# Performance work log

Hardware: AMD Instinct MI355X
Metric: run time of the kernel (lower is better)

## Reference

```python
import jax, jax.numpy as jnp
import numpy as np

D_MODEL = 1024
N_HEADS = 8
HEAD_DIM = D_MODEL // N_HEADS
B, T = 4, 2048


def setup_inputs() -> dict:
    key = jax.random.key(0)
    ks = jax.random.split(key, 10)
    x = jax.random.normal(ks[0], (B, T, D_MODEL), dtype=jnp.float32)
    # causal mask: True entries are masked (matches torch masked_fill semantics)
    mask = jnp.triu(jnp.ones((T, T), dtype=bool), k=1)

    def xavier(k, shape):
        fan_in, fan_out = shape[1], shape[0]
        lim = float(np.sqrt(6.0 / (fan_in + fan_out)))
        return jax.random.uniform(k, shape, jnp.float32, -lim, lim)

    Wq = xavier(ks[1], (D_MODEL, D_MODEL)); bq = jnp.zeros((D_MODEL,), jnp.float32)
    Wk = xavier(ks[2], (D_MODEL, D_MODEL)); bk = jnp.zeros((D_MODEL,), jnp.float32)
    Wv = xavier(ks[3], (D_MODEL, D_MODEL)); bv = jnp.zeros((D_MODEL,), jnp.float32)
    Wo = xavier(ks[4], (D_MODEL, D_MODEL)); bo = jnp.zeros((D_MODEL,), jnp.float32)
    return {"x": x, "mask": mask, "Wq": Wq, "bq": bq, "Wk": Wk, "bk": bk,
            "Wv": Wv, "bv": bv, "Wo": Wo, "bo": bo}


def reference(x, mask, Wq, bq, Wk, bk, Wv, bv, Wo, bo):
    Bsz, Tlen, _ = x.shape
    # torch Linear: y = x @ W.T + b
    Q = (x @ Wq.T + bq).reshape(Bsz, Tlen, N_HEADS, HEAD_DIM).transpose(0, 2, 1, 3)  # [B,H,T,Dh]
    K = (x @ Wk.T + bk).reshape(Bsz, Tlen, N_HEADS, HEAD_DIM).transpose(0, 2, 1, 3)  # [B,H,T,Dh]
    V_shared = x @ Wv.T + bv  # [B,T,D] shared across heads
    scale = 1.0 / jnp.sqrt(jnp.float32(HEAD_DIM))
    scores = jnp.einsum('bhqd,bhkd->bhqk', Q, K) * scale  # [B,H,T,T]
    scores = jnp.where(mask[None, None, :, :], jnp.float32(-1e9), scores)
    attn_per_head = jax.nn.softmax(scores, axis=-1)
    alpha_agg = attn_per_head.mean(axis=1)  # [B,T,T] head-averaged attention
    out = jnp.einsum('bqk,bkd->bqd', alpha_agg, V_shared) @ Wo.T + bo
    return out, alpha_agg
```

## Files before the change

### kernel.cpp

```cpp
#include <hip/hip_runtime.h>
#include <hip/hip_bf16.h>

#define D_MODEL 1024
#define NH 8
#define HD 128
#define BATCH 4
#define TSEQ 2048
#define MROWS (BATCH * TSEQ)
#define QKV_LD 3072

typedef __attribute__((ext_vector_type(8))) __bf16 bf16x8;
typedef __attribute__((ext_vector_type(4))) __bf16 bf16x4;
typedef __attribute__((ext_vector_type(4))) float f32x4;
typedef __attribute__((ext_vector_type(8))) unsigned short u16x8;

#define SC2 0.1275174441680632f

__device__ __forceinline__ void gload16(const void* g, void* lds) {
  __builtin_amdgcn_global_load_lds(
      (const __attribute__((address_space(1))) unsigned int*)g,
      (__attribute__((address_space(3))) unsigned int*)lds, 16, 0, 0);
}

__global__ __launch_bounds__(256) void cvt_f32_to_bf16(const float* __restrict__ in,
                                                       __bf16* __restrict__ out, int n4) {
  int i = blockIdx.x * 256 + threadIdx.x;
  if (i < n4) {
    float4 v = reinterpret_cast<const float4*>(in)[i];
    bf16x4 o;
    o[0] = (__bf16)v.x; o[1] = (__bf16)v.y; o[2] = (__bf16)v.z; o[3] = (__bf16)v.w;
    reinterpret_cast<bf16x4*>(out)[i] = o;
  }
}

__global__ __launch_bounds__(256) void cvt4_weights(const float* __restrict__ w0,
                                                    const float* __restrict__ w1,
                                                    const float* __restrict__ w2,
                                                    const float* __restrict__ w3,
                                                    __bf16* __restrict__ out) {
  const int per = D_MODEL * D_MODEL / 4;
  int i = blockIdx.x * 256 + threadIdx.x;
  int m = i / per, j = i - m * per;
  const float* src = (m == 0) ? w0 : (m == 1) ? w1 : (m == 2) ? w2 : w3;
  float4 v = reinterpret_cast<const float4*>(src)[j];
  bf16x4 o;
  o[0] = (__bf16)v.x; o[1] = (__bf16)v.y; o[2] = (__bf16)v.z; o[3] = (__bf16)v.w;
  reinterpret_cast<bf16x4*>(out)[i] = o;
}

__global__ __launch_bounds__(256) void concat_bias(const float* __restrict__ a,
                                                   const float* __restrict__ b,
                                                   const float* __restrict__ c,
                                                   float* __restrict__ o) {
  int i = blockIdx.x * 256 + threadIdx.x;
  if (i < 3072) o[i] = (i < 1024) ? a[i] : (i < 2048) ? b[i - 1024] : c[i - 2048];
}

__global__ __launch_bounds__(256) void invert_lsum(float* __restrict__ L, int n) {
  int i = blockIdx.x * 256 + threadIdx.x;
  if (i < n) L[i] = 1.0f / (8.0f * L[i]);
}

template <bool BF16OUT, bool CAUSAL, bool AFP32>
__global__ __launch_bounds__(256) void gemm128(const void* __restrict__ Aip,
                                               const __bf16* __restrict__ Bp,
                                               const float* __restrict__ bias,
                                               void* __restrict__ Yp, int K, int ldy,
                                               size_t sA, size_t sB, size_t sY) {
  __shared__ __bf16 As[2][128 * 32];
  __shared__ __bf16 Bs[2][128 * 32];
  const int tid = threadIdx.x;
  const int w = tid >> 6, l = tid & 63;
  const int lr = l & 15, lg = l >> 4;
  const int m0 = blockIdx.y * 128, n0 = blockIdx.x * 128;
  const int z = blockIdx.z;
  const __bf16* Ab = AFP32 ? nullptr : (const __bf16*)Aip + z * sA;
  const float* Af = AFP32 ? (const float*)Aip + z * sA : nullptr;
  const __bf16* Bb = Bp + z * sB;
  const int wm = w >> 1, wn = w & 1;
  f32x4 acc[4][4] = {};
  const int Klim = CAUSAL ? (m0 + 128 < K ? m0 + 128 : K) : K;
  const int nt = Klim >> 5;

  auto stage = [&](int t, int buf) {
    const int k0 = t << 5;
    if constexpr (!AFP32) {
#pragma unroll
      for (int i = 0; i < 2; ++i) {
        int s = w * 128 + i * 64 + l;
        int row = s >> 2, scp = s & 3;
        int sc = scp ^ ((row >> 1) & 3);
        gload16(Ab + (size_t)(m0 + row) * K + k0 + sc * 8, (char*)As[buf] + s * 16);
      }
    } else {
#pragma unroll
      for (int i = 0; i < 2; ++i) {
        int s = w * 128 + i * 64 + l;
        int row = s >> 2, sc = s & 3;
        const float* src = Af + (size_t)(m0 + row) * K + k0 + sc * 8;
        float4 lo = *reinterpret_cast<const float4*>(src);
        float4 hi = *reinterpret_cast<const float4*>(src + 4);
        bf16x8 v;
        v[0] = (__bf16)lo.x; v[1] = (__bf16)lo.y; v[2] = (__bf16)lo.z; v[3] = (__bf16)lo.w;
        v[4] = (__bf16)hi.x; v[5] = (__bf16)hi.y; v[6] = (__bf16)hi.z; v[7] = (__bf16)hi.w;
        int p = row * 4 + (sc ^ ((row >> 1) & 3));
        *reinterpret_cast<bf16x8*>((char*)As[buf] + p * 16) = v;
      }
    }
#pragma unroll
    for (int i = 0; i < 2; ++i) {
      int s = w * 128 + i * 64 + l;
      int row = s >> 2, scp = s & 3;
      int sc = scp ^ ((row >> 1) & 3);
      gload16(Bb + (size_t)(n0 + row) * K + k0 + sc * 8, (char*)Bs[buf] + s * 16);
    }
  };

  stage(0, 0);
  __syncthreads();
  int cur = 0;
  for (int t = 0; t < nt; ++t) {
    if (t + 1 < nt) stage(t + 1, cur ^ 1);
    bf16x8 af[4], bf[4];
#pragma unroll
    for (int f = 0; f < 4; ++f) {
      int ar = wm * 64 + f * 16 + lr;
      af[f] = *reinterpret_cast<const bf16x8*>((const char*)As[cur] + ar * 64 +
                                               ((lg ^ ((ar >> 1) & 3)) * 16));
      int br = wn * 64 + f * 16 + lr;
      bf[f] = *reinterpret_cast<const bf16x8*>((const char*)Bs[cur] + br * 64 +
                                               ((lg ^ ((br >> 1) & 3)) * 16));
    }
#pragma unroll
    for (int mf = 0; mf < 4; ++mf)
#pragma unroll
      for (int nf = 0; nf < 4; ++nf)
        acc[mf][nf] = __builtin_amdgcn_mfma_f32_16x16x32_bf16(af[mf], bf[nf], acc[mf][nf], 0, 0, 0);
    __syncthreads();
    cur ^= 1;
  }

#pragma unroll
  for (int mf = 0; mf < 4; ++mf) {
#pragma unroll
    for (int nf = 0; nf < 4; ++nf) {
#pragma unroll
      for (int r = 0; r < 4; ++r) {
        int grow = m0 + wm * 64 + mf * 16 + lg * 4 + r;
        int gcol = n0 + wn * 64 + nf * 16 + lr;
        float v = acc[mf][nf][r];
        if (bias) v += bias[gcol];
        if constexpr (BF16OUT)
          ((__bf16*)Yp + z * sY)[(size_t)grow * ldy + gcol] = (__bf16)v;
        else
          ((float*)Yp + z * sY)[(size_t)grow * ldy + gcol] = v;
      }
    }
  }
}

__global__ __launch_bounds__(256) void transpose_v(const __bf16* __restrict__ V,
                                                   __bf16* __restrict__ Vt) {
  __shared__ unsigned short tile[64 * 72];
  const int b = blockIdx.z;
  const int t0 = blockIdx.x * 64, d0 = blockIdx.y * 64;
  const int tid = threadIdx.x;
#pragma unroll
  for (int i = 0; i < 2; ++i) {
    int s = i * 256 + tid;
    int r = s >> 3, c8 = s & 7;
    u16x8 v = *reinterpret_cast<const u16x8*>(V + ((size_t)b * TSEQ + t0 + r) * QKV_LD + d0 + c8 * 8);
    *reinterpret_cast<u16x8*>(&tile[r * 72 + c8 * 8]) = v;
  }
  __syncthreads();
#pragma unroll
  for (int i = 0; i < 2; ++i) {
    int s = i * 256 + tid;
    int dr = s >> 3, t8 = s & 7;
    u16x8 o;
#pragma unroll
    for (int j = 0; j < 8; ++j) o[j] = tile[(t8 * 8 + j) * 72 + dr];
    *reinterpret_cast<u16x8*>(Vt + ((size_t)b * D_MODEL + d0 + dr) * TSEQ + t0 + t8 * 8) = o;
  }
}

__device__ __forceinline__ void stage_tile128(const __bf16* __restrict__ src,
                                              __bf16* __restrict__ dst, int tid, int ld) {
#pragma unroll
  for (int i = 0; i < 4; ++i) {
    int s = i * 512 + tid;
    int row = s >> 4, sp = s & 15;
    int sl = sp ^ (row & 15);
    gload16(src + (size_t)row * ld + sl * 8, (char*)dst + s * 16);
  }
}

__device__ __forceinline__ bf16x8 ldfrag(const __bf16* t, int row, int c, int lg) {
  return *reinterpret_cast<const bf16x8*>((const char*)t + row * 256 +
                                          (((c * 4 + lg) ^ (row & 15)) * 16));
}

template <int MODE>
__global__ __launch_bounds__(512) void attn128(const __bf16* __restrict__ QKV,
                                               const float* __restrict__ Linv,
                                               float* __restrict__ Out) {
  const int kt = blockIdx.x, qt = blockIdx.y, b = blockIdx.z;
  const int tid = threadIdx.x;
  const int q0 = qt * 128, k0 = kt * 128;
  if (kt > qt) {
    if (MODE == 1) {
      float4 zz = {0.f, 0.f, 0.f, 0.f};
#pragma unroll
      for (int i = 0; i < 8; ++i) {
        int s = i * 512 + tid;
        int row = s >> 5, c = s & 31;
        *reinterpret_cast<float4*>(Out + ((size_t)(b * TSEQ) + q0 + row) * TSEQ + k0 + c * 4) = zz;
      }
    }
    return;
  }
  __shared__ __bf16 Qs[2][128 * 128];
  __shared__ __bf16 Ks[2][128 * 128];
  const int w = tid >> 6, l = tid & 63;
  const int lr = l & 15, lg = l >> 4;
  const int wq = w >> 1;
  const int wk = w & 1;
  const __bf16* qb0 = QKV + (size_t)(b * TSEQ + q0) * QKV_LD;
  const __bf16* kb0 = QKV + (size_t)(b * TSEQ + k0) * QKV_LD + 1024;

  stage_tile128(qb0, Qs[0], tid, QKV_LD);
  stage_tile128(kb0, Ks[0], tid, QKV_LD);
  __syncthreads();

  float outv[2][4][4] = {};
  int cur = 0;
  for (int h = 0; h < NH; ++h) {
    if (h + 1 < NH) {
      stage_tile128(qb0 + (h + 1) * HD, Qs[cur ^ 1], tid, QKV_LD);
      stage_tile128(kb0 + (h + 1) * HD, Ks[cur ^ 1], tid, QKV_LD);
    }
    bf16x8 af[2][4], bf[4][4];
#pragma unroll
    for (int mf = 0; mf < 2; ++mf)
#pragma unroll
      for (int c = 0; c < 4; ++c) af[mf][c] = ldfrag(Qs[cur], wq * 32 + mf * 16 + lr, c, lg);
#pragma unroll
    for (int nf = 0; nf < 4; ++nf)
#pragma unroll
      for (int c = 0; c < 4; ++c) bf[nf][c] = ldfrag(Ks[cur], wk * 64 + nf * 16 + lr, c, lg);
    f32x4 acc[2][4] = {};
#pragma unroll
    for (int c = 0; c < 4; ++c)
#pragma unroll
      for (int mf = 0; mf < 2; ++mf)
#pragma unroll
        for (int nf = 0; nf < 4; ++nf)
          acc[mf][nf] = __builtin_amdgcn_mfma_f32_16x16x32_bf16(af[mf][c], bf[nf][c], acc[mf][nf], 0, 0, 0);

    if constexpr (MODE == 0) {
      float ls[2][4] = {};
#pragma unroll
      for (int mf = 0; mf < 2; ++mf)
#pragma unroll
        for (int nf = 0; nf < 4; ++nf)
#pragma unroll
          for (int r = 0; r < 4; ++r) {
            int q = q0 + wq * 32 + mf * 16 + lg * 4 + r;
            int k = k0 + wk * 64 + nf * 16 + lr;
            if (kt < qt || k <= q) ls[mf][r] += exp2f(acc[mf][nf][r] * SC2);
          }
#pragma unroll
      for (int m = 1; m < 16; m <<= 1)
#pragma unroll
        for (int mf = 0; mf < 2; ++mf)
#pragma unroll
          for (int r = 0; r < 4; ++r) ls[mf][r] += __shfl_xor(ls[mf][r], m, 64);
      if (lr == 0) {
#pragma unroll
        for (int mf = 0; mf < 2; ++mf)
#pragma unroll
          for (int r = 0; r < 4; ++r)
            atomicAdd(&Out[((size_t)(b * NH + h)) * TSEQ + q0 + wq * 32 + mf * 16 + lg * 4 + r],
                      ls[mf][r]);
      }
    } else {
      float4 li[2];
#pragma unroll
      for (int mf = 0; mf < 2; ++mf)
        li[mf] = *reinterpret_cast<const float4*>(
            &Linv[((size_t)(b * NH + h)) * TSEQ + q0 + wq * 32 + mf * 16 + lg * 4]);
#pragma unroll
      for (int mf = 0; mf < 2; ++mf)
#pragma unroll
        for (int nf = 0; nf < 4; ++nf)
#pragma unroll
          for (int r = 0; r < 4; ++r) {
            int q = q0 + wq * 32 + mf * 16 + lg * 4 + r;
            int k = k0 + wk * 64 + nf * 16 + lr;
            if (kt < qt || k <= q)
              outv[mf][nf][r] += exp2f(acc[mf][nf][r] * SC2) * (&li[mf].x)[r];
          }
    }
    __syncthreads();
    cur ^= 1;
  }
  if constexpr (MODE == 1) {
#pragma unroll
    for (int mf = 0; mf < 2; ++mf)
#pragma unroll
      for (int nf = 0; nf < 4; ++nf)
#pragma unroll
        for (int r = 0; r < 4; ++r)
          Out[((size_t)(b * TSEQ) + q0 + wq * 32 + mf * 16 + lg * 4 + r) * TSEQ +
              k0 + wk * 64 + nf * 16 + lr] = outv[mf][nf][r];
  }
}

extern "C" void kernel_launch(void* const* d_in, const int* in_sizes, int n_in,
                              void* d_out, int out_size, void* d_ws, size_t ws_size,
                              hipStream_t stream) {
  const float* x  = (const float*)d_in[0];
  const float* Wq = (const float*)d_in[2];
  const float* bq = (const float*)d_in[3];
  const float* Wk = (const float*)d_in[4];
  const float* bk = (const float*)d_in[5];
  const float* Wv = (const float*)d_in[6];
  const float* bv = (const float*)d_in[7];
  const float* Wo = (const float*)d_in[8];
  const float* bo = (const float*)d_in[9];

  float* out_f = (float*)d_out;
  float* alpha = out_f + (size_t)MROWS * D_MODEL;

  char* p = (char*)d_ws;
  __bf16* xb   = (__bf16*)p; p += (size_t)MROWS * D_MODEL * 2;
  __bf16* wqb  = (__bf16*)p; p += (size_t)D_MODEL * D_MODEL * 2;
  __bf16* wkb  = (__bf16*)p; p += (size_t)D_MODEL * D_MODEL * 2;
  __bf16* wvb  = (__bf16*)p; p += (size_t)D_MODEL * D_MODEL * 2;
  __bf16* wob  = (__bf16*)p; p += (size_t)D_MODEL * D_MODEL * 2;
  __bf16* qkv  = (__bf16*)p; p += (size_t)MROWS * QKV_LD * 2;
  __bf16* vtb  = (__bf16*)p; p += (size_t)BATCH * D_MODEL * TSEQ * 2;
  float* lsum  = (float*)p;  p += (size_t)BATCH * NH * TSEQ * 4;
  float* bcat  = (float*)p;  p += 3072 * 4;
  __bf16* midb = xb;

  hipMemsetAsync(lsum, 0, (size_t)BATCH * NH * TSEQ * 4, stream);

  {
    int n4 = MROWS * D_MODEL / 4;
    cvt_f32_to_bf16<<<n4 / 256, 256, 0, stream>>>(x, xb, n4);
    int w4 = 4 * D_MODEL * D_MODEL / 4;
    cvt4_weights<<<w4 / 256, 256, 0, stream>>>(Wq, Wk, Wv, Wo, wqb);
    concat_bias<<<12, 256, 0, stream>>>(bq, bk, bv, bcat);
  }

  gemm128<true, false, false><<<dim3(QKV_LD / 128, MROWS / 128), 256, 0, stream>>>(
      xb, wqb, bcat, qkv, D_MODEL, QKV_LD, 0, 0, 0);

  transpose_v<<<dim3(TSEQ / 64, D_MODEL / 64, BATCH), 256, 0, stream>>>(qkv + 2048, vtb);

  attn128<0><<<dim3(TSEQ / 128, TSEQ / 128, BATCH), 512, 0, stream>>>(qkv, nullptr, lsum);
  invert_lsum<<<(BATCH * NH * TSEQ) / 256, 256, 0, stream>>>(lsum, BATCH * NH * TSEQ);

  attn128<1><<<dim3(TSEQ / 128, TSEQ / 128, BATCH), 512, 0, stream>>>(qkv, lsum, alpha);

  gemm128<true, true, true><<<dim3(D_MODEL / 128, TSEQ / 128, BATCH), 256, 0, stream>>>(
      alpha, vtb, nullptr, midb, TSEQ, D_MODEL,
      (size_t)TSEQ * TSEQ, (size_t)D_MODEL * TSEQ, (size_t)TSEQ * D_MODEL);

  gemm128<false, false, false><<<dim3(D_MODEL / 128, MROWS / 128), 256, 0, stream>>>(
      midb, wob, bo, out_f, D_MODEL, D_MODEL, 0, 0, 0);
}
```

Before: 393.5 us.

## Restructure attention score kernels to 4 waves with 64-wide K-chunk staging

The attention score kernels now run with 256 threads (4 waves) instead of 512. Each wave computes a 64x64 tile, so there are more MFMAs per fragment load. Staging switches from full 128-wide head tiles to 64-column chunks, cutting LDS use from 128KB to 64KB, which may allow more blocks per CU. Accumulators persist across two chunks per head and are reset after the softmax or normalization step. The cost is higher register pressure from the 4x4 accumulators plus the outv array, which could hurt occupancy.

```diff
diff --git a/kernel.cpp b/kernel.cpp
--- a/kernel.cpp
+++ b/kernel.cpp
@@ -184,26 +184,26 @@
   }
 }
 
-__device__ __forceinline__ void stage_tile128(const __bf16* __restrict__ src,
-                                              __bf16* __restrict__ dst, int tid, int ld) {
+__device__ __forceinline__ void stage64(const __bf16* __restrict__ src,
+                                        __bf16* __restrict__ dst, int tid) {
 #pragma unroll
   for (int i = 0; i < 4; ++i) {
-    int s = i * 512 + tid;
-    int row = s >> 4, sp = s & 15;
-    int sl = sp ^ (row & 15);
-    gload16(src + (size_t)row * ld + sl * 8, (char*)dst + s * 16);
-  }
-}
-
-__device__ __forceinline__ bf16x8 ldfrag(const __bf16* t, int row, int c, int lg) {
-  return *reinterpret_cast<const bf16x8*>((const char*)t + row * 256 +
-                                          (((c * 4 + lg) ^ (row & 15)) * 16));
+    int s = i * 256 + tid;
+    int row = s >> 3, sp = s & 7;
+    int sl = sp ^ (row & 7);
+    gload16(src + (size_t)row * QKV_LD + sl * 8, (char*)dst + s * 16);
+  }
+}
+
+__device__ __forceinline__ bf16x8 ldfrag64(const __bf16* t, int row, int c, int lg) {
+  return *reinterpret_cast<const bf16x8*>((const char*)t + row * 128 +
+                                          (((c * 4 + lg) ^ (row & 7)) * 16));
 }
 
 template <int MODE>
-__global__ __launch_bounds__(512) void attn128(const __bf16* __restrict__ QKV,
-                                               const float* __restrict__ Linv,
-                                               float* __restrict__ Out) {
+__global__ __launch_bounds__(256) void attn4w(const __bf16* __restrict__ QKV,
+                                              const float* __restrict__ Linv,
+                                              float* __restrict__ Out) {
   const int kt = blockIdx.x, qt = blockIdx.y, b = blockIdx.z;
   const int tid = threadIdx.x;
   const int q0 = qt * 128, k0 = kt * 128;
@@ -211,107 +211,115 @@
     if (MODE == 1) {
       float4 zz = {0.f, 0.f, 0.f, 0.f};
 #pragma unroll
-      for (int i = 0; i < 8; ++i) {
-        int s = i * 512 + tid;
+      for (int i = 0; i < 16; ++i) {
+        int s = i * 256 + tid;
         int row = s >> 5, c = s & 31;
         *reinterpret_cast<float4*>(Out + ((size_t)(b * TSEQ) + q0 + row) * TSEQ + k0 + c * 4) = zz;
       }
     }
     return;
   }
-  __shared__ __bf16 Qs[2][128 * 128];
-  __shared__ __bf16 Ks[2][128 * 128];
+  __shared__ __bf16 Qs[2][128 * 64];
+  __shared__ __bf16 Ks[2][128 * 64];
   const int w = tid >> 6, l = tid & 63;
   const int lr = l & 15, lg = l >> 4;
-  const int wq = w >> 1;
-  const int wk = w & 1;
+  const int wq = w >> 1, wk = w & 1;
   const __bf16* qb0 = QKV + (size_t)(b * TSEQ + q0) * QKV_LD;
   const __bf16* kb0 = QKV + (size_t)(b * TSEQ + k0) * QKV_LD + 1024;
 
-  stage_tile128(qb0, Qs[0], tid, QKV_LD);
-  stage_tile128(kb0, Ks[0], tid, QKV_LD);
+  stage64(qb0, Qs[0], tid);
+  stage64(kb0, Ks[0], tid);
   __syncthreads();
 
-  float outv[2][4][4] = {};
+  f32x4 acc[4][4] = {};
+  float outv[4][4][4] = {};
+  float li[4][4];
   int cur = 0;
-  for (int h = 0; h < NH; ++h) {
-    if (h + 1 < NH) {
-      stage_tile128(qb0 + (h + 1) * HD, Qs[cur ^ 1], tid, QKV_LD);
-      stage_tile128(kb0 + (h + 1) * HD, Ks[cur ^ 1], tid, QKV_LD);
-    }
-    bf16x8 af[2][4], bf[4][4];
-#pragma unroll
-    for (int mf = 0; mf < 2; ++mf)
-#pragma unroll
-      for (int c = 0; c < 4; ++c) af[mf][c] = ldfrag(Qs[cur], wq * 32 + mf * 16 + lr, c, lg);
-#pragma unroll
-    for (int nf = 0; nf < 4; ++nf)
-#pragma unroll
-      for (int c = 0; c < 4; ++c) bf[nf][c] = ldfrag(Ks[cur], wk * 64 + nf * 16 + lr, c, lg);
-    f32x4 acc[2][4] = {};
-#pragma unroll
-    for (int c = 0; c < 4; ++c)
-#pragma unroll
-      for (int mf = 0; mf < 2; ++mf)
+#pragma unroll 1
+  for (int t = 0; t < 16; ++t) {
+    if (t < 15) {
+      stage64(qb0 + (t + 1) * 64, Qs[cur ^ 1], tid);
+      stage64(kb0 + (t + 1) * 64, Ks[cur ^ 1], tid);
+    }
+    if (MODE == 1 && (t & 1) == 0) {
+      int h = t >> 1;
+#pragma unroll
+      for (int mf = 0; mf < 4; ++mf) {
+        float4 v = *reinterpret_cast<const float4*>(
+            &Linv[((size_t)(b * NH + h)) * TSEQ + q0 + wq * 64 + mf * 16 + lg * 4]);
+        li[mf][0] = v.x; li[mf][1] = v.y; li[mf][2] = v.z; li[mf][3] = v.w;
+      }
+    }
+#pragma unroll
+    for (int c = 0; c < 2; ++c) {
+      bf16x8 af[4], bf[4];
+#pragma unroll
+      for (int f = 0; f < 4; ++f) {
+        af[f] = ldfrag64(Qs[cur], wq * 64 + f * 16 + lr, c, lg);
+        bf[f] = ldfrag64(Ks[cur], wk * 64 + f * 16 + lr, c, lg);
+      }
+#pragma unroll
+      for (int mf = 0; mf < 4; ++mf)
 #pragma unroll
         for (int nf = 0; nf < 4; ++nf)
-          acc[mf][nf] = __builtin_amdgcn_mfma_f32_16x16x32_bf16(af[mf][c], bf[nf][c], acc[mf][nf], 0, 0, 0);
-
-    if constexpr (MODE == 0) {
-      float ls[2][4] = {};
-#pragma unroll
-      for (int mf = 0; mf < 2; ++mf)
-#pragma unroll
-        for (int nf = 0; nf < 4; ++nf)
-#pragma unroll
-          for (int r = 0; r < 4; ++r) {
-            int q = q0 + wq * 32 + mf * 16 + lg * 4 + r;
-            int k = k0 + wk * 64 + nf * 16 + lr;
-            if (kt < qt || k <= q) ls[mf][r] += exp2f(acc[mf][nf][r] * SC2);
-          }
-#pragma unroll
-      for (int m = 1; m < 16; m <<= 1)
-#pragma unroll
-        for (int mf = 0; mf < 2; ++mf)
-#pragma unroll
-          for (int r = 0; r < 4; ++r) ls[mf][r] += __shfl_xor(ls[mf][r], m, 64);
-      if (lr == 0) {
-#pragma unroll
-        for (int mf = 0; mf < 2; ++mf)
-#pragma unroll
-          for (int r = 0; r < 4; ++r)
-            atomicAdd(&Out[((size_t)(b * NH + h)) * TSEQ + q0 + wq * 32 + mf * 16 + lg * 4 + r],
-                      ls[mf][r]);
-      }
-    } else {
-      float4 li[2];
-#pragma unroll
-      for (int mf = 0; mf < 2; ++mf)
-        li[mf] = *reinterpret_cast<const float4*>(
-            &Linv[((size_t)(b * NH + h)) * TSEQ + q0 + wq * 32 + mf * 16 + lg * 4]);
-#pragma unroll
-      for (int mf = 0; mf < 2; ++mf)
-#pragma unroll
-        for (int nf = 0; nf < 4; ++nf)
-#pragma unroll
-          for (int r = 0; r < 4; ++r) {
-            int q = q0 + wq * 32 + mf * 16 + lg * 4 + r;
-            int k = k0 + wk * 64 + nf * 16 + lr;
-            if (kt < qt || k <= q)
-              outv[mf][nf][r] += exp2f(acc[mf][nf][r] * SC2) * (&li[mf].x)[r];
-          }
+          acc[mf][nf] = __builtin_amdgcn_mfma_f32_16x16x32_bf16(af[mf], bf[nf], acc[mf][nf], 0, 0, 0);
+    }
+    if (t & 1) {
+      const int h = t >> 1;
+      const bool diag = (kt == qt);
+      if constexpr (MODE == 0) {
+        float ls[4][4] = {};
+#pragma unroll
+        for (int mf = 0; mf < 4; ++mf)
+#pragma unroll
+          for (int nf = 0; nf < 4; ++nf)
+#pragma unroll
+            for (int r = 0; r < 4; ++r) {
+              int q = wq * 64 + mf * 16 + lg * 4 + r;
+              int k = wk * 64 + nf * 16 + lr;
+              if (!diag || k <= q) ls[mf][r] += exp2f(acc[mf][nf][r] * SC2);
+              acc[mf][nf][r] = 0.f;
+            }
+#pragma unroll
+        for (int m = 1; m < 16; m <<= 1)
+#pragma unroll
+          for (int mf = 0; mf < 4; ++mf)
+#pragma unroll
+            for (int r = 0; r < 4; ++r) ls[mf][r] += __shfl_xor(ls[mf][r], m, 64);
+        if (lr == 0) {
+#pragma unroll
+          for (int mf = 0; mf < 4; ++mf)
+#pragma unroll
+            for (int r = 0; r < 4; ++r)
+              atomicAdd(&Out[((size_t)(b * NH + h)) * TSEQ + q0 + wq * 64 + mf * 16 + lg * 4 + r],
+                        ls[mf][r]);
+        }
+      } else {
+#pragma unroll
+        for (int mf = 0; mf < 4; ++mf)
+#pragma unroll
+          for (int nf = 0; nf < 4; ++nf)
+#pragma unroll
+            for (int r = 0; r < 4; ++r) {
+              int q = wq * 64 + mf * 16 + lg * 4 + r;
+              int k = wk * 64 + nf * 16 + lr;
+              if (!diag || k <= q)
+                outv[mf][nf][r] += exp2f(acc[mf][nf][r] * SC2) * li[mf][r];
+              acc[mf][nf][r] = 0.f;
+            }
+      }
     }
     __syncthreads();
     cur ^= 1;
   }
   if constexpr (MODE == 1) {
 #pragma unroll
-    for (int mf = 0; mf < 2; ++mf)
+    for (int mf = 0; mf < 4; ++mf)
 #pragma unroll
       for (int nf = 0; nf < 4; ++nf)
 #pragma unroll
         for (int r = 0; r < 4; ++r)
-          Out[((size_t)(b * TSEQ) + q0 + wq * 32 + mf * 16 + lg * 4 + r) * TSEQ +
+          Out[((size_t)(b * TSEQ) + q0 + wq * 64 + mf * 16 + lg * 4 + r) * TSEQ +
               k0 + wk * 64 + nf * 16 + lr] = outv[mf][nf][r];
   }
 }
@@ -359,10 +367,10 @@
 
   transpose_v<<<dim3(TSEQ / 64, D_MODEL / 64, BATCH), 256, 0, stream>>>(qkv + 2048, vtb);
 
-  attn128<0><<<dim3(TSEQ / 128, TSEQ / 128, BATCH), 512, 0, stream>>>(qkv, nullptr, lsum);
+  attn4w<0><<<dim3(TSEQ / 128, TSEQ / 128, BATCH), 256, 0, stream>>>(qkv, nullptr, lsum);
   invert_lsum<<<(BATCH * NH * TSEQ) / 256, 256, 0, stream>>>(lsum, BATCH * NH * TSEQ);
 
-  attn128<1><<<dim3(TSEQ / 128, TSEQ / 128, BATCH), 512, 0, stream>>>(qkv, lsum, alpha);
+  attn4w<1><<<dim3(TSEQ / 128, TSEQ / 128, BATCH), 256, 0, stream>>>(qkv, lsum, alpha);
 
   gemm128<true, true, true><<<dim3(D_MODEL / 128, TSEQ / 128, BATCH), 256, 0, stream>>>(
       alpha, vtb, nullptr, midb, TSEQ, D_MODEL,
```

Measured after the change: 510.8 us. +29.8%, slower.

## Stage attention Q/K in 32-wide k-slices to shrink LDS and raise occupancy

Applied to the files above, without the earlier changes.

The attention score kernels now stream Q and K in 32-column slices (one 16-byte load per thread per slice) instead of staging a full 128x128 head tile per head. This cuts shared memory from 128KB to 32KB and sets launch bounds to allow four blocks per CU. Accumulators are carried across four slices per head, and the exp/normalise step runs every fourth iteration. In exchange there are many more barriers (32 per block instead of 8) and less load latency is hidden per stage.

```diff
diff --git a/kernel.cpp b/kernel.cpp
--- a/kernel.cpp
+++ b/kernel.cpp
@@ -184,29 +184,13 @@
   }
 }
 
-__device__ __forceinline__ void stage_tile128(const __bf16* __restrict__ src,
-                                              __bf16* __restrict__ dst, int tid, int ld) {
-#pragma unroll
-  for (int i = 0; i < 4; ++i) {
-    int s = i * 512 + tid;
-    int row = s >> 4, sp = s & 15;
-    int sl = sp ^ (row & 15);
-    gload16(src + (size_t)row * ld + sl * 8, (char*)dst + s * 16);
-  }
-}
-
-__device__ __forceinline__ bf16x8 ldfrag(const __bf16* t, int row, int c, int lg) {
-  return *reinterpret_cast<const bf16x8*>((const char*)t + row * 256 +
-                                          (((c * 4 + lg) ^ (row & 15)) * 16));
-}
-
 template <int MODE>
-__global__ __launch_bounds__(512) void attn128(const __bf16* __restrict__ QKV,
-                                               const float* __restrict__ Linv,
-                                               float* __restrict__ Out) {
+__global__ __launch_bounds__(512, 4) void attn8w(const __bf16* __restrict__ QKV,
+                                                 const float* __restrict__ Linv,
+                                                 float* __restrict__ Out) {
   const int kt = blockIdx.x, qt = blockIdx.y, b = blockIdx.z;
+  const int q0 = qt * 128, k0 = kt * 128;
   const int tid = threadIdx.x;
-  const int q0 = qt * 128, k0 = kt * 128;
   if (kt > qt) {
     if (MODE == 1) {
       float4 zz = {0.f, 0.f, 0.f, 0.f};
@@ -219,100 +203,113 @@
     }
     return;
   }
-  __shared__ __bf16 Qs[2][128 * 128];
-  __shared__ __bf16 Ks[2][128 * 128];
+  __shared__ __bf16 As[2][128 * 32];
+  __shared__ __bf16 Bs[2][128 * 32];
   const int w = tid >> 6, l = tid & 63;
   const int lr = l & 15, lg = l >> 4;
-  const int wq = w >> 1;
-  const int wk = w & 1;
-  const __bf16* qb0 = QKV + (size_t)(b * TSEQ + q0) * QKV_LD;
-  const __bf16* kb0 = QKV + (size_t)(b * TSEQ + k0) * QKV_LD + 1024;
-
-  stage_tile128(qb0, Qs[0], tid, QKV_LD);
-  stage_tile128(kb0, Ks[0], tid, QKV_LD);
+  const int wq = w >> 1, wk = w & 1;
+  const __bf16* Qb = QKV + (size_t)(b * TSEQ + q0) * QKV_LD;
+  const __bf16* Kb = QKV + (size_t)(b * TSEQ + k0) * QKV_LD + 1024;
+  const int srow = tid >> 2, ssl = (tid & 3) ^ ((srow >> 1) & 3);
+  const __bf16* qsrc = Qb + (size_t)srow * QKV_LD + ssl * 8;
+  const __bf16* ksrc = Kb + (size_t)srow * QKV_LD + ssl * 8;
+
+  gload16(qsrc, (char*)As[0] + tid * 16);
+  gload16(ksrc, (char*)Bs[0] + tid * 16);
   __syncthreads();
 
+  f32x4 acc[2][4] = {};
   float outv[2][4][4] = {};
+  const bool diag = (kt == qt);
   int cur = 0;
-  for (int h = 0; h < NH; ++h) {
-    if (h + 1 < NH) {
-      stage_tile128(qb0 + (h + 1) * HD, Qs[cur ^ 1], tid, QKV_LD);
-      stage_tile128(kb0 + (h + 1) * HD, Ks[cur ^ 1], tid, QKV_LD);
-    }
-    bf16x8 af[2][4], bf[4][4];
-#pragma unroll
-    for (int mf = 0; mf < 2; ++mf)
-#pragma unroll
-      for (int c = 0; c < 4; ++c) af[mf][c] = ldfrag(Qs[cur], wq * 32 + mf * 16 + lr, c, lg);
-#pragma unroll
-    for (int nf = 0; nf < 4; ++nf)
-#pragma unroll
-      for (int c = 0; c < 4; ++c) bf[nf][c] = ldfrag(Ks[cur], wk * 64 + nf * 16 + lr, c, lg);
-    f32x4 acc[2][4] = {};
-#pragma unroll
-    for (int c = 0; c < 4; ++c)
-#pragma unroll
-      for (int mf = 0; mf < 2; ++mf)
-#pragma unroll
-        for (int nf = 0; nf < 4; ++nf)
-          acc[mf][nf] = __builtin_amdgcn_mfma_f32_16x16x32_bf16(af[mf][c], bf[nf][c], acc[mf][nf], 0, 0, 0);
-
-    if constexpr (MODE == 0) {
-      float ls[2][4] = {};
-#pragma unroll
-      for (int mf = 0; mf < 2; ++mf)
-#pragma unroll
-        for (int nf = 0; nf < 4; ++nf)
-#pragma unroll
-          for (int r = 0; r < 4; ++r) {
-            int q = q0 + wq * 32 + mf * 16 + lg * 4 + r;
-            int k = k0 + wk * 64 + nf * 16 + lr;
-            if (kt < qt || k <= q) ls[mf][r] += exp2f(acc[mf][nf][r] * SC2);
-          }
-#pragma unroll
-      for (int m = 1; m < 16; m <<= 1)
-#pragma unroll
-        for (int mf = 0; mf < 2; ++mf)
-#pragma unroll
-          for (int r = 0; r < 4; ++r) ls[mf][r] += __shfl_xor(ls[mf][r], m, 64);
-      if (lr == 0) {
-#pragma unroll
-        for (int mf = 0; mf < 2; ++mf)
-#pragma unroll
-          for (int r = 0; r < 4; ++r)
-            atomicAdd(&Out[((size_t)(b * NH + h)) * TSEQ + q0 + wq * 32 + mf * 16 + lg * 4 + r],
-                      ls[mf][r]);
-      }
-    } else {
-      float4 li[2];
-#pragma unroll
-      for (int mf = 0; mf < 2; ++mf)
-        li[mf] = *reinterpret_cast<const float4*>(
-            &Linv[((size_t)(b * NH + h)) * TSEQ + q0 + wq * 32 + mf * 16 + lg * 4]);
-#pragma unroll
-      for (int mf = 0; mf < 2; ++mf)
-#pragma unroll
-        for (int nf = 0; nf < 4; ++nf)
-#pragma unroll
-          for (int r = 0; r < 4; ++r) {
-            int q = q0 + wq * 32 + mf * 16 + lg * 4 + r;
-            int k = k0 + wk * 64 + nf * 16 + lr;
-            if (kt < qt || k <= q)
-              outv[mf][nf][r] += exp2f(acc[mf][nf][r] * SC2) * (&li[mf].x)[r];
-          }
+#pragma unroll 1
+  for (int t = 0; t < 32; ++t) {
+    if (t < 31) {
+      gload16(qsrc + (t + 1) * 32, (char*)As[cur ^ 1] + tid * 16);
+      gload16(ksrc + (t + 1) * 32, (char*)Bs[cur ^ 1] + tid * 16);
+    }
+    bf16x8 af[2], bf[4];
+#pragma unroll
+    for (int f = 0; f < 2; ++f) {
+      int ar = wq * 32 + f * 16 + lr;
+      af[f] = *reinterpret_cast<const bf16x8*>((const char*)As[cur] + ar * 64 +
+                                               ((lg ^ ((ar >> 1) & 3)) * 16));
+    }
+#pragma unroll
+    for (int g = 0; g < 4; ++g) {
+      int br = wk * 64 + g * 16 + lr;
+      bf[g] = *reinterpret_cast<const bf16x8*>((const char*)Bs[cur] + br * 64 +
+                                               ((lg ^ ((br >> 1) & 3)) * 16));
+    }
+#pragma unroll
+    for (int f = 0; f < 2; ++f)
+#pragma unroll
+      for (int g = 0; g < 4; ++g)
+        acc[f][g] = __builtin_amdgcn_mfma_f32_16x16x32_bf16(af[f], bf[g], acc[f][g], 0, 0, 0);
+
+    if ((t & 3) == 3) {
+      const int h = t >> 2;
+      if constexpr (MODE == 0) {
+        float ls[2][4] = {};
+#pragma unroll
+        for (int f = 0; f < 2; ++f)
+#pragma unroll
+          for (int g = 0; g < 4; ++g)
+#pragma unroll
+            for (int r = 0; r < 4; ++r) {
+              int q = wq * 32 + f * 16 + lg * 4 + r;
+              int k = wk * 64 + g * 16 + lr;
+              if (!diag || k <= q) ls[f][r] += exp2f(acc[f][g][r] * SC2);
+              acc[f][g][r] = 0.f;
+            }
+#pragma unroll
+        for (int m = 1; m < 16; m <<= 1)
+#pragma unroll
+          for (int f = 0; f < 2; ++f)
+#pragma unroll
+            for (int r = 0; r < 4; ++r) ls[f][r] += __shfl_xor(ls[f][r], m, 64);
+        if (lr == 0) {
+#pragma unroll
+          for (int f = 0; f < 2; ++f)
+#pragma unroll
+            for (int r = 0; r < 4; ++r)
+              atomicAdd(&Out[((size_t)(b * NH + h)) * TSEQ + q0 + wq * 32 + f * 16 + lg * 4 + r],
+                        ls[f][r]);
+        }
+      } else {
+        float li[2][4];
+#pragma unroll
+        for (int f = 0; f < 2; ++f) {
+          float4 v = *reinterpret_cast<const float4*>(
+              &Linv[((size_t)(b * NH + h)) * TSEQ + q0 + wq * 32 + f * 16 + lg * 4]);
+          li[f][0] = v.x; li[f][1] = v.y; li[f][2] = v.z; li[f][3] = v.w;
+        }
+#pragma unroll
+        for (int f = 0; f < 2; ++f)
+#pragma unroll
+          for (int g = 0; g < 4; ++g)
+#pragma unroll
+            for (int r = 0; r < 4; ++r) {
+              int q = wq * 32 + f * 16 + lg * 4 + r;
+              int k = wk * 64 + g * 16 + lr;
+              if (!diag || k <= q)
+                outv[f][g][r] += exp2f(acc[f][g][r] * SC2) * li[f][r];
+              acc[f][g][r] = 0.f;
+            }
+      }
     }
     __syncthreads();
     cur ^= 1;
   }
   if constexpr (MODE == 1) {
 #pragma unroll
-    for (int mf = 0; mf < 2; ++mf)
-#pragma unroll
-      for (int nf = 0; nf < 4; ++nf)
+    for (int f = 0; f < 2; ++f)
+#pragma unroll
+      for (int g = 0; g < 4; ++g)
 #pragma unroll
         for (int r = 0; r < 4; ++r)
-          Out[((size_t)(b * TSEQ) + q0 + wq * 32 + mf * 16 + lg * 4 + r) * TSEQ +
-              k0 + wk * 64 + nf * 16 + lr] = outv[mf][nf][r];
+          Out[((size_t)(b * TSEQ) + q0 + wq * 32 + f * 16 + lg * 4 + r) * TSEQ +
+              k0 + wk * 64 + g * 16 + lr] = outv[f][g][r];
   }
 }
 
@@ -359,10 +356,10 @@
 
   transpose_v<<<dim3(TSEQ / 64, D_MODEL / 64, BATCH), 256, 0, stream>>>(qkv + 2048, vtb);
 
-  attn128<0><<<dim3(TSEQ / 128, TSEQ / 128, BATCH), 512, 0, stream>>>(qkv, nullptr, lsum);
+  attn8w<0><<<dim3(TSEQ / 128, TSEQ / 128, BATCH), 512, 0, stream>>>(qkv, nullptr, lsum);
   invert_lsum<<<(BATCH * NH * TSEQ) / 256, 256, 0, stream>>>(lsum, BATCH * NH * TSEQ);
 
-  attn128<1><<<dim3(TSEQ / 128, TSEQ / 128, BATCH), 512, 0, stream>>>(qkv, lsum, alpha);
+  attn8w<1><<<dim3(TSEQ / 128, TSEQ / 128, BATCH), 512, 0, stream>>>(qkv, lsum, alpha);
 
   gemm128<true, true, true><<<dim3(D_MODEL / 128, TSEQ / 128, BATCH), 256, 0, stream>>>(
       alpha, vtb, nullptr, midb, TSEQ, D_MODEL,
```

Measured after the change: 375.2 us. 1.05x faster.
